# Kernel tuning notes

Hardware: AMD Instinct MI355X
Metric: run time of the kernel (lower is better)

Reference implementation:

```python
import jax, jax.numpy as jnp
import numpy as np

B, T, N, FI = 2, 16, 256, 1
H, NHEAD, L = 64, 4, 2
MID, LOW, FOUT = 32, 16, 1


def layer_norm(x, g, b, eps=1e-5):
    m = jnp.mean(x, axis=-1, keepdims=True)
    v = jnp.var(x, axis=-1, keepdims=True)
    return (x - m) / jnp.sqrt(v + eps) * g + b


def setup_inputs() -> dict:
    key = jax.random.key(0)
    ks = jax.random.split(key, 24)
    s = 0.05
    inp = {
        'x_seq': jax.random.normal(ks[0], (B, T, N, FI), jnp.float32),
        'edge_index': jax.random.randint(ks[1], (2, 16), 0, N),
        'Wi': jax.random.normal(ks[2], (FI, H), jnp.float32) * s,
        'bi': jnp.zeros((H,), jnp.float32),
        'Wqkv': jax.random.normal(ks[3], (L, H, 3 * H), jnp.float32) * s,
        'bqkv': jnp.zeros((L, 3 * H), jnp.float32),
        'Wo': jax.random.normal(ks[4], (L, H, H), jnp.float32) * s,
        'bo': jnp.zeros((L, H), jnp.float32),
        'ln1_g': jnp.ones((L, H), jnp.float32),
        'ln1_b': jnp.zeros((L, H), jnp.float32),
        'W1': jax.random.normal(ks[5], (L, H, 4 * H), jnp.float32) * s,
        'b1': jnp.zeros((L, 4 * H), jnp.float32),
        'W2': jax.random.normal(ks[6], (L, 4 * H, H), jnp.float32) * s,
        'b2': jnp.zeros((L, H), jnp.float32),
        'ln2_g': jnp.ones((L, H), jnp.float32),
        'ln2_b': jnp.zeros((L, H), jnp.float32),
        'dW1': jax.random.normal(ks[7], (H, MID), jnp.float32) * s,
        'db1': jnp.zeros((MID,), jnp.float32),
        'dW2': jax.random.normal(ks[8], (MID, LOW), jnp.float32) * s,
        'db2': jnp.zeros((LOW,), jnp.float32),
        'dW3': jax.random.normal(ks[9], (LOW, FOUT), jnp.float32) * s,
        'db3': jnp.zeros((FOUT,), jnp.float32),
    }
    return inp


def reference(x_seq, edge_index, Wi, bi, Wqkv, bqkv, Wo, bo, ln1_g, ln1_b,
              W1, b1, W2, b2, ln2_g, ln2_b, dW1, db1, dW2, db2, dW3, db3):
    b, t, n, _ = x_seq.shape
    dh = H // NHEAD
    # input projection
    x = x_seq @ Wi + bi  # [B,T,N,H]
    # sinusoidal time positional encoding (broadcast over nodes)
    pos = jnp.arange(t, dtype=jnp.float32)[:, None]
    div = jnp.exp(jnp.arange(0, H, 2, dtype=jnp.float32) * (-jnp.log(10000.0) / H))
    tp = jnp.zeros((t, H), jnp.float32)
    tp = tp.at[:, 0::2].set(jnp.sin(pos * div)).at[:, 1::2].set(jnp.cos(pos * div))
    x = x + tp[None, :, None, :]
    S = t * n
    x = x.reshape(b, S, H)
    # block-causal additive bias: position i cannot attend to strictly future timesteps
    t_idx = jnp.arange(S) // n
    bias = jnp.where(t_idx[None, :] > t_idx[:, None], -jnp.inf, 0.0).astype(x.dtype)
    inv_sqrt_dh = 1.0 / jnp.sqrt(jnp.asarray(dh, x.dtype))
    for l in range(L):
        qkv = x @ Wqkv[l] + bqkv[l]  # [B,S,3H]
        q, k, v = jnp.split(qkv, 3, axis=-1)
        q = q.reshape(b, S, NHEAD, dh).transpose(0, 2, 1, 3)
        k = k.reshape(b, S, NHEAD, dh).transpose(0, 2, 1, 3)
        v = v.reshape(b, S, NHEAD, dh).transpose(0, 2, 1, 3)
        scores = jnp.einsum('bhqd,bhkd->bhqk', q, k) * inv_sqrt_dh + bias
        attn = jax.nn.softmax(scores, axis=-1)
        o = jnp.einsum('bhqk,bhkd->bhqd', attn, v)
        o = o.transpose(0, 2, 1, 3).reshape(b, S, H)
        o = o @ Wo[l] + bo[l]
        x = layer_norm(x + o, ln1_g[l], ln1_b[l])
        f = jax.nn.relu(x @ W1[l] + b1[l]) @ W2[l] + b2[l]
        x = layer_norm(x + f, ln2_g[l], ln2_b[l])
    last = x.reshape(b, t, n, H)[:, -1]  # [B,N,H]
    h = jax.nn.relu(last @ dW1 + db1)
    h = jax.nn.relu(h @ dW2 + db2)
    return h @ dW3 + db3  # [B,N,1]
```

## Files before the change

kernel.cpp:

```cpp
#include <hip/hip_runtime.h>
#include <math.h>


namespace {
constexpr int T_ = 16, N_ = 256, S_ = 4096;
constexpr int PAIRS = 136;

constexpr size_t OFF_A    = 0;
constexpr size_t OFF_BT   = 192;
constexpr size_t OFF_XB   = 3264;
constexpr size_t OFF_ALPH = 4288;
constexpr size_t OFF_BET  = 4292;
constexpr size_t OFF_GAM  = 4356;
constexpr size_t OFF_DELT = 4420;
constexpr size_t OFF_MN   = 5444;
constexpr size_t OFF_MX   = 5476;
constexpr size_t OFF_X    = 5632;
constexpr size_t OFF_QKV  = 529920;
constexpr size_t OFF_P0   = 2102784;
constexpr size_t OFF_PM1  = 3675648;
constexpr size_t OFF_PL1  = 3708416;
constexpr size_t OFF_PA1  = 3741184;

typedef float  f32x16 __attribute__((ext_vector_type(16)));
typedef short  short8 __attribute__((ext_vector_type(8)));

__device__ inline float wave_sum(float v) {
#pragma unroll
  for (int off = 32; off > 0; off >>= 1) v += __shfl_xor(v, off, 64);
  return v;
}
__device__ inline unsigned bf16_rne(float f) {
  unsigned u = __float_as_uint(f);
  return (u + 0x7FFFu + ((u >> 16) & 1u)) >> 16;
}
__device__ inline unsigned pack2(float a, float b) {
  return bf16_rne(a) | (bf16_rne(b) << 16);
}
__device__ inline f32x16 zero16() {
  f32x16 z;
#pragma unroll
  for (int i = 0; i < 16; ++i) z[i] = 0.f;
  return z;
}
__device__ inline float pe_val(int t, int h) {
  float div = __expf((float)(h & ~1) * (-0.14391156831212787f));
  float arg = (float)t * div;
  return (h & 1) ? cosf(arg) : sinf(arg);
}

__global__ void k_setup(const float* __restrict__ x_seq,
                        const float* __restrict__ Wi, const float* __restrict__ bi,
                        const float* __restrict__ Wqkv, const float* __restrict__ bqkv,
                        float* __restrict__ A, float* __restrict__ Bt,
                        float* __restrict__ Xb,
                        float* __restrict__ ALPH, float* __restrict__ BET,
                        float* __restrict__ GAM, float* __restrict__ DELT,
                        float* __restrict__ MN, float* __restrict__ MX) {
  int t = blockIdx.x, tid = threadIdx.x;
  if (t < 16) {
    if (tid < 192) {
      float acc = bqkv[tid];
#pragma unroll 8
      for (int h = 0; h < 64; ++h)
        acc = fmaf(bi[h] + pe_val(t, h), Wqkv[h * 192 + tid], acc);
      Bt[t * 192 + tid] = acc;
    }
    if (tid < 64) Xb[t * 64 + tid] = bi[tid] + pe_val(t, tid);
  } else if (t == 16) {
    if (tid < 192) {
      float acc = 0.f;
#pragma unroll 8
      for (int h = 0; h < 64; ++h) acc = fmaf(Wi[h], Wqkv[h * 192 + tid], acc);
      A[tid] = acc;
    }
  } else if (t == 17) {
    __shared__ float sA[128];
    __shared__ float sB[16][128];
    if (tid < 128) {
      float acc = 0.f;
#pragma unroll 8
      for (int h = 0; h < 64; ++h) acc = fmaf(Wi[h], Wqkv[h * 192 + tid], acc);
      sA[tid] = acc;
    }
    {
      int tt = tid >> 4, i = tid & 15;
      float accv[8];
#pragma unroll
      for (int j = 0; j < 8; ++j) accv[j] = bqkv[i * 8 + j];
      for (int h = 0; h < 64; ++h) {
        float xb = bi[h] + pe_val(tt, h);
#pragma unroll
        for (int j = 0; j < 8; ++j)
          accv[j] = fmaf(xb, Wqkv[h * 192 + i * 8 + j], accv[j]);
      }
#pragma unroll
      for (int j = 0; j < 8; ++j) sB[tt][i * 8 + j] = accv[j];
    }
    __syncthreads();
    const float k2 = 0.36067376022224085f;
    if (tid < 4) {
      float d = 0.f;
#pragma unroll
      for (int i = 0; i < 16; ++i) d = fmaf(sA[tid * 16 + i], sA[64 + tid * 16 + i], d);
      ALPH[tid] = k2 * d;
    }
    if (tid < 64) {
      int h = tid >> 4, tp2 = tid & 15;
      float d = 0.f, g = 0.f;
#pragma unroll
      for (int i = 0; i < 16; ++i) {
        d = fmaf(sA[h * 16 + i], sB[tp2][64 + h * 16 + i], d);
        g = fmaf(sA[64 + h * 16 + i], sB[tp2][h * 16 + i], g);
      }
      BET[h * 16 + tp2] = k2 * d;
      GAM[h * 16 + tp2] = k2 * g;
    }
#pragma unroll
    for (int q = 0; q < 4; ++q) {
      int idx = tid + 256 * q;
      int h = idx >> 8, ta = (idx >> 4) & 15, tb = idx & 15;
      float d = 0.f;
#pragma unroll
      for (int i = 0; i < 16; ++i)
        d = fmaf(sB[ta][h * 16 + i], sB[tb][64 + h * 16 + i], d);
      DELT[h * 256 + ta * 16 + tb] = k2 * d;
    }
  } else {
    int g = tid >> 3, i = tid & 7;
    const float* xp = x_seq + (g >> 4) * S_ + (g & 15) * N_;
    float mn = 1e30f, mx = -1e30f;
    for (int j = i; j < 256; j += 8) {
      float v = xp[j];
      mn = fminf(mn, v); mx = fmaxf(mx, v);
    }
#pragma unroll
    for (int off = 1; off < 8; off <<= 1) {
      mn = fminf(mn, __shfl_xor(mn, off, 64));
      mx = fmaxf(mx, __shfl_xor(mx, off, 64));
    }
    if (i == 0) { MN[g] = mn; MX[g] = mx; }
  }
}

__global__ __launch_bounds__(256, 4) void k_attn0(
    const float* __restrict__ x_seq,
    const float* __restrict__ ALPH, const float* __restrict__ BET,
    const float* __restrict__ GAM, const float* __restrict__ DELT,
    const float* __restrict__ MN, const float* __restrict__ MX,
    float* __restrict__ P0) {
  __shared__ float4 xk4[64];
  int blk = blockIdx.x;
  int bh = blk / PAIRS, pair = blk % PAIRS;
  int b = bh >> 2, h = bh & 3;
  int tq = 0, p = pair;
  while (p >= tq + 1) { p -= tq + 1; ++tq; }
  int kt = p;
  int tid = threadIdx.x;
  if (tid < 64) xk4[tid] = *(const float4*)(x_seq + (size_t)(b * S_ + kt * N_) + 4 * tid);
  __syncthreads();

  float x = x_seq[b * S_ + tq * N_ + tid];
  float a = fmaf(ALPH[h], x, GAM[h * 16 + tq]);
  float xext = (a >= 0.f) ? MX[b * 16 + kt] : MN[b * 16 + kt];
  float axext = a * xext;
  float Mg = axext + fmaf(BET[h * 16 + kt], x, DELT[h * 256 + tq * 16 + kt]);
  float sp0 = 0.f, sp1 = 0.f, sp2 = 0.f, sp3 = 0.f;
  float sx0 = 0.f, sx1 = 0.f, sx2 = 0.f, sx3 = 0.f;
#pragma unroll 8
  for (int j = 0; j < 64; ++j) {
    float4 xv = xk4[j];
    float e0 = __builtin_amdgcn_exp2f(fmaf(a, xv.x, -axext));
    float e1 = __builtin_amdgcn_exp2f(fmaf(a, xv.y, -axext));
    float e2 = __builtin_amdgcn_exp2f(fmaf(a, xv.z, -axext));
    float e3 = __builtin_amdgcn_exp2f(fmaf(a, xv.w, -axext));
    sp0 += e0; sp1 += e1; sp2 += e2; sp3 += e3;
    sx0 = fmaf(xv.x, e0, sx0); sx1 = fmaf(xv.y, e1, sx1);
    sx2 = fmaf(xv.z, e2, sx2); sx3 = fmaf(xv.w, e3, sx3);
  }
  size_t pb = ((size_t)(bh * 16 + tq) * 16 + kt) * 768;
  P0[pb + tid]       = Mg;
  P0[pb + 256 + tid] = (sp0 + sp1) + (sp2 + sp3);
  P0[pb + 512 + tid] = (sx0 + sx1) + (sx2 + sx3);
}

__global__ __launch_bounds__(256, 4) void k_fused0(
    const float* __restrict__ P0, const float* __restrict__ A,
    const float* __restrict__ Bt, const float* __restrict__ Xb,
    const float* __restrict__ x_seq, const float* __restrict__ Wi,
    const float* __restrict__ Wo, const float* __restrict__ bo,
    const float* __restrict__ g1, const float* __restrict__ be1,
    const float* __restrict__ W1, const float* __restrict__ bb1,
    const float* __restrict__ W2, const float* __restrict__ bb2,
    const float* __restrict__ g2, const float* __restrict__ be2,
    const float* __restrict__ Wq1, const float* __restrict__ bq1,
    float* __restrict__ X, float* __restrict__ QKV) {
  __shared__ float os[8][64], rs[8][64], xs[8][64], x2[8][64], hs[8][256];
  int tid = threadIdx.x;
  int row0 = blockIdx.x * 8;
  int b = row0 >> 12, t = (row0 >> 8) & 15, n0 = row0 & 255;

  {
    int r = tid & 7, h = (tid >> 3) & 3, d2 = tid >> 5;
    int n = n0 + r, bh = b * 4 + h;
    float M = -INFINITY, D = 0.f, SX = 0.f, bacc0 = 0.f, bacc1 = 0.f;
    for (int kt = 0; kt <= t; ++kt) {
      size_t pb = ((size_t)(bh * 16 + t) * 16 + kt) * 768 + n;
      float mg = P0[pb], sp = P0[pb + 256], sx = P0[pb + 512];
      float mnv = fmaxf(M, mg);
      float sc = __builtin_amdgcn_exp2f(M - mnv);
      float w  = __builtin_amdgcn_exp2f(mg - mnv);
      float wsp = w * sp;
      D  = fmaf(w, sp, D * sc);
      SX = fmaf(w, sx, SX * sc);
      float2 bv = *(const float2*)(Bt + kt * 192 + 128 + h * 16 + d2 * 2);
      bacc0 = fmaf(wsp, bv.x, bacc0 * sc);
      bacc1 = fmaf(wsp, bv.y, bacc1 * sc);
      M = mnv;
    }
    float invD = 1.f / D;
    float2 av = *(const float2*)(A + 128 + h * 16 + d2 * 2);
    os[r][h * 16 + d2 * 2 + 0] = fmaf(SX, av.x, bacc0) * invD;
    os[r][h * 16 + d2 * 2 + 1] = fmaf(SX, av.y, bacc1) * invD;
  }
  {
    int idx = tid;
#pragma unroll
    for (int i = 0; i < 2; ++i, idx += 256) {
      int r = idx >> 6, cc = idx & 63;
      rs[r][cc] = fmaf(x_seq[row0 + r], Wi[cc], Xb[t * 64 + cc]);
    }
  }
  __syncthreads();

  int c = tid & 63, grp = tid >> 6;
#pragma unroll
  for (int rr = 0; rr < 2; ++rr) {
    int r = grp + 4 * rr;
    float a = bo[c];
#pragma unroll 8
    for (int k = 0; k < 64; ++k) a = fmaf(os[r][k], Wo[k * 64 + c], a);
    float val = a + rs[r][c];
    float mean = wave_sum(val) * (1.f / 64.f);
    float dv = val - mean;
    float var = wave_sum(dv * dv) * (1.f / 64.f);
    xs[r][c] = dv * rsqrtf(var + 1e-5f) * g1[c] + be1[c];
  }
  __syncthreads();

  {
    float am[8];
#pragma unroll
    for (int i = 0; i < 8; ++i) am[i] = bb1[tid];
    for (int k4 = 0; k4 < 16; ++k4) {
      float w0 = W1[(4 * k4 + 0) * 256 + tid];
      float w1v = W1[(4 * k4 + 1) * 256 + tid];
      float w2v = W1[(4 * k4 + 2) * 256 + tid];
      float w3v = W1[(4 * k4 + 3) * 256 + tid];
#pragma unroll
      for (int r = 0; r < 8; ++r) {
        float4 xv = *(const float4*)&xs[r][4 * k4];
        am[r] = fmaf(xv.x, w0, am[r]);
        am[r] = fmaf(xv.y, w1v, am[r]);
        am[r] = fmaf(xv.z, w2v, am[r]);
        am[r] = fmaf(xv.w, w3v, am[r]);
      }
    }
#pragma unroll
    for (int r = 0; r < 8; ++r) hs[r][tid] = fmaxf(am[r], 0.f);
  }
  __syncthreads();

  {
    float a0 = bb2[c], a1 = bb2[c];
    for (int k4 = 0; k4 < 64; ++k4) {
      float w0 = W2[(4 * k4 + 0) * 64 + c];
      float w1v = W2[(4 * k4 + 1) * 64 + c];
      float w2v = W2[(4 * k4 + 2) * 64 + c];
      float w3v = W2[(4 * k4 + 3) * 64 + c];
      float4 h0 = *(const float4*)&hs[grp][4 * k4];
      float4 h1 = *(const float4*)&hs[grp + 4][4 * k4];
      a0 = fmaf(h0.x, w0, a0); a0 = fmaf(h0.y, w1v, a0);
      a0 = fmaf(h0.z, w2v, a0); a0 = fmaf(h0.w, w3v, a0);
      a1 = fmaf(h1.x, w0, a1); a1 = fmaf(h1.y, w1v, a1);
      a1 = fmaf(h1.z, w2v, a1); a1 = fmaf(h1.w, w3v, a1);
    }
    float av[2] = {a0, a1};
#pragma unroll
    for (int rr = 0; rr < 2; ++rr) {
      int r = grp + 4 * rr;
      float val = av[rr] + xs[r][c];
      float mean = wave_sum(val) * (1.f / 64.f);
      float dv = val - mean;
      float var = wave_sum(dv * dv) * (1.f / 64.f);
      float xn = dv * rsqrtf(var + 1e-5f) * g2[c] + be2[c];
      x2[r][c] = xn;
      if (t == 15) X[(size_t)(row0 + r) * 64 + c] = xn;
    }
  }
  __syncthreads();

  {
    int ncol = (t == 15) ? 192 : 128;
    int cb = (t == 15) ? 0 : 64;
    if (tid < ncol) {
      int col = cb + tid;
      float acc[8];
#pragma unroll
      for (int r = 0; r < 8; ++r) acc[r] = bq1[col];
      for (int k4 = 0; k4 < 16; ++k4) {
        float w0 = Wq1[(4 * k4 + 0) * 192 + col];
        float w1v = Wq1[(4 * k4 + 1) * 192 + col];
        float w2v = Wq1[(4 * k4 + 2) * 192 + col];
        float w3v = Wq1[(4 * k4 + 3) * 192 + col];
#pragma unroll
        for (int r = 0; r < 8; ++r) {
          float4 xv = *(const float4*)&x2[r][4 * k4];
          acc[r] = fmaf(xv.x, w0, acc[r]);
          acc[r] = fmaf(xv.y, w1v, acc[r]);
          acc[r] = fmaf(xv.z, w2v, acc[r]);
          acc[r] = fmaf(xv.w, w3v, acc[r]);
        }
      }
#pragma unroll
      for (int r = 0; r < 8; ++r)
        QKV[(size_t)(row0 + r) * 192 + col] = acc[r];
    }
  }
}

__global__ __launch_bounds__(256, 4) void k_attn1(const float* __restrict__ QKV,
    float* __restrict__ PM, float* __restrict__ PL, float* __restrict__ PACC) {
  __shared__ short KH[2][256][8];
  __shared__ short KL[2][256][8];
  __shared__ short VT[32][264];
  int blk = blockIdx.x;
  int bh = blk >> 4, kt = blk & 15;
  const int tq = 15;
  int b = bh >> 2, h = bh & 3;
  int tid = threadIdx.x, w = tid >> 6, lane = tid & 63;
  int l31 = lane & 31, hi = lane >> 5;
  const size_t qkvbase = (size_t)b * S_ * 192;

  for (int i = tid; i < 16 * 264; i += 256) (&VT[16][0])[i] = 0;
  {
    const float* kp = QKV + qkvbase + (size_t)(kt * N_ + tid) * 192 + 64 + h * 16;
    float kf[16], vf[16];
#pragma unroll
    for (int i = 0; i < 4; ++i) {
      float4 k4 = *(const float4*)(kp + 4 * i);
      kf[4 * i] = k4.x; kf[4 * i + 1] = k4.y; kf[4 * i + 2] = k4.z; kf[4 * i + 3] = k4.w;
      float4 v4 = *(const float4*)(kp + 64 + 4 * i);
      vf[4 * i] = v4.x; vf[4 * i + 1] = v4.y; vf[4 * i + 2] = v4.z; vf[4 * i + 3] = v4.w;
    }
    short8 kh0, kh1, kl0, kl1;
#pragma unroll
    for (int i = 0; i < 8; ++i) {
      unsigned ht0 = __float_as_uint(kf[i]) & 0xFFFF0000u;
      kh0[i] = (short)(ht0 >> 16);
      kl0[i] = (short)bf16_rne(kf[i] - __uint_as_float(ht0));
      unsigned ht1 = __float_as_uint(kf[i + 8]) & 0xFFFF0000u;
      kh1[i] = (short)(ht1 >> 16);
      kl1[i] = (short)bf16_rne(kf[i + 8] - __uint_as_float(ht1));
    }
    *(short8*)&KH[0][tid][0] = kh0;
    *(short8*)&KH[1][tid][0] = kh1;
    *(short8*)&KL[0][tid][0] = kl0;
    *(short8*)&KL[1][tid][0] = kl1;
#pragma unroll
    for (int i = 0; i < 16; ++i) VT[i][tid] = (short)bf16_rne(vf[i]);
  }
  __syncthreads();

  const float cscale = 0.36067376022224085f;
  short8 Qh[2], Ql[2];
#pragma unroll
  for (int qs = 0; qs < 2; ++qs) {
    int qloc = w * 64 + qs * 32 + l31;
    const float* qp = QKV + qkvbase + (size_t)(tq * N_ + qloc) * 192 + h * 16 + 8 * hi;
    float4 a4 = *(const float4*)(qp), b4 = *(const float4*)(qp + 4);
    float qf[8] = {a4.x, a4.y, a4.z, a4.w, b4.x, b4.y, b4.z, b4.w};
#pragma unroll
    for (int i = 0; i < 8; ++i) {
      float q = qf[i] * cscale;
      unsigned ht = __float_as_uint(q) & 0xFFFF0000u;
      Qh[qs][i] = (short)(ht >> 16);
      Ql[qs][i] = (short)bf16_rne(q - __uint_as_float(ht));
    }
  }

  f32x16 O0 = zero16(), O1 = zero16();
  float m[2] = {-INFINITY, -INFINITY}, lsum[2] = {0.f, 0.f};

  for (int ks = 0; ks < 8; ++ks) {
    const short8 Kh = *(const short8*)&KH[hi][ks * 32 + l31][0];
    const short8 Kl = *(const short8*)&KL[hi][ks * 32 + l31][0];
    const short8 Va = *(const short8*)&VT[l31][ks * 32 + 8 * hi];
    const short8 Vb = *(const short8*)&VT[l31][ks * 32 + 8 * hi + 16];

#pragma unroll
    for (int qs = 0; qs < 2; ++qs) {
      f32x16 S = zero16();
      S = __builtin_amdgcn_mfma_f32_32x32x16_bf16(Kh, Qh[qs], S, 0, 0, 0);
      S = __builtin_amdgcn_mfma_f32_32x32x16_bf16(Kl, Qh[qs], S, 0, 0, 0);
      S = __builtin_amdgcn_mfma_f32_32x32x16_bf16(Kh, Ql[qs], S, 0, 0, 0);

      float pm = S[0];
#pragma unroll
      for (int r = 1; r < 16; ++r) pm = fmaxf(pm, S[r]);
      pm = fmaxf(pm, __shfl_xor(pm, 32, 64));
      float mq = m[qs];
      if (__any(pm > mq)) {
        float mn = fmaxf(mq, pm);
        float al = __builtin_amdgcn_exp2f(mq - mn);
        m[qs] = mn; mq = mn;
        lsum[qs] *= al;
        if (qs == 0) {
#pragma unroll
          for (int r = 0; r < 16; ++r) O0[r] *= al;
        } else {
#pragma unroll
          for (int r = 0; r < 16; ++r) O1[r] *= al;
        }
      }
      float pr[16], ps = 0.f;
#pragma unroll
      for (int r = 0; r < 16; ++r) {
        pr[r] = __builtin_amdgcn_exp2f(S[r] - mq);
        ps += pr[r];
      }
      lsum[qs] += ps + __shfl_xor(ps, 32, 64);

      unsigned w01 = pack2(pr[0],  pr[1]);
      unsigned w23 = pack2(pr[2],  pr[3]);
      unsigned w45 = pack2(pr[4],  pr[5]);
      unsigned w67 = pack2(pr[6],  pr[7]);
      unsigned w89 = pack2(pr[8],  pr[9]);
      unsigned wab = pack2(pr[10], pr[11]);
      unsigned wcd = pack2(pr[12], pr[13]);
      unsigned wef = pack2(pr[14], pr[15]);
      unsigned e01 = __shfl_xor(w01, 32, 64), e23 = __shfl_xor(w23, 32, 64);
      unsigned e45 = __shfl_xor(w45, 32, 64), e67 = __shfl_xor(w67, 32, 64);
      unsigned e89 = __shfl_xor(w89, 32, 64), eab = __shfl_xor(wab, 32, 64);
      unsigned ecd = __shfl_xor(wcd, 32, 64), eef = __shfl_xor(wef, 32, 64);
      union { short8 s; unsigned u[4]; } P0u, P1u;
      P0u.u[0] = hi ? e45 : w01;
      P0u.u[1] = hi ? e67 : w23;
      P0u.u[2] = hi ? w45 : e01;
      P0u.u[3] = hi ? w67 : e23;
      P1u.u[0] = hi ? ecd : w89;
      P1u.u[1] = hi ? eef : wab;
      P1u.u[2] = hi ? wcd : e89;
      P1u.u[3] = hi ? wef : eab;

      if (qs == 0) {
        O0 = __builtin_amdgcn_mfma_f32_32x32x16_bf16(Va, P0u.s, O0, 0, 0, 0);
        O0 = __builtin_amdgcn_mfma_f32_32x32x16_bf16(Vb, P1u.s, O0, 0, 0, 0);
      } else {
        O1 = __builtin_amdgcn_mfma_f32_32x32x16_bf16(Va, P0u.s, O1, 0, 0, 0);
        O1 = __builtin_amdgcn_mfma_f32_32x32x16_bf16(Vb, P1u.s, O1, 0, 0, 0);
      }
    }
  }

  int slot = blk;
#pragma unroll
  for (int qs = 0; qs < 2; ++qs) {
    int qloc = w * 64 + qs * 32 + l31;
    if (lane < 32) {
      PM[(size_t)slot * 256 + qloc] = m[qs];
      PL[(size_t)slot * 256 + qloc] = lsum[qs];
    }
    float* pa = PACC + (size_t)slot * 4096 + (size_t)qloc * 16;
    float4 lo4, hi4;
    if (qs == 0) {
      lo4 = make_float4(O0[0], O0[1], O0[2], O0[3]);
      hi4 = make_float4(O0[4], O0[5], O0[6], O0[7]);
    } else {
      lo4 = make_float4(O1[0], O1[1], O1[2], O1[3]);
      hi4 = make_float4(O1[4], O1[5], O1[6], O1[7]);
    }
    *(float4*)(pa + 4 * hi)     = lo4;
    *(float4*)(pa + 8 + 4 * hi) = hi4;
  }
}

__global__ __launch_bounds__(256, 2) void k_fused1(
    const float* __restrict__ PM1, const float* __restrict__ PL1,
    const float* __restrict__ PA1,
    const float* __restrict__ Wo, const float* __restrict__ bo,
    const float* __restrict__ g1, const float* __restrict__ be1,
    const float* __restrict__ W1, const float* __restrict__ bb1,
    const float* __restrict__ W2, const float* __restrict__ bb2,
    const float* __restrict__ g2, const float* __restrict__ be2,
    const float* __restrict__ X,
    const float* __restrict__ dW1, const float* __restrict__ db1,
    const float* __restrict__ dW2, const float* __restrict__ db2,
    const float* __restrict__ dW3, const float* __restrict__ db3,
    float* __restrict__ out) {
  __shared__ float os[4][64], rs[4][64], xs[4][64], x2[4][64], hs[4][256];
  __shared__ float h1s[4][32], h2s[4][16];
  int tid = threadIdx.x;
  int bb = blockIdx.x >> 6;
  int nbase = (blockIdx.x & 63) * 4;
  int row0 = bb * S_ + 15 * N_ + nbase;
  size_t base = (size_t)row0 * 64;

  {
    int d = tid & 15, r = (tid >> 4) & 3, h = tid >> 6;
    int n = nbase + r;
    int sb = (bb * 4 + h) * 16;
    float M = -INFINITY;
#pragma unroll
    for (int s = 0; s < 16; ++s) M = fmaxf(M, PM1[(size_t)(sb + s) * 256 + n]);
    float D = 0.f, od = 0.f;
#pragma unroll
    for (int s = 0; s < 16; ++s) {
      float wgt = __builtin_amdgcn_exp2f(PM1[(size_t)(sb + s) * 256 + n] - M);
      D = fmaf(PL1[(size_t)(sb + s) * 256 + n], wgt, D);
      od = fmaf(PA1[(size_t)(sb + s) * 4096 + (size_t)n * 16 + d], wgt, od);
    }
    os[r][h * 16 + d] = od / D;
    rs[tid >> 6][tid & 63] = X[base + tid];
  }
  __syncthreads();

  int c = tid & 63, grp = tid >> 6;
  {
    float a = bo[c];
#pragma unroll 8
    for (int k = 0; k < 64; ++k) a = fmaf(os[grp][k], Wo[k * 64 + c], a);
    float val = a + rs[grp][c];
    float mean = wave_sum(val) * (1.f / 64.f);
    float dv = val - mean;
    float var = wave_sum(dv * dv) * (1.f / 64.f);
    xs[grp][c] = dv * rsqrtf(var + 1e-5f) * g1[c] + be1[c];
  }
  __syncthreads();

  {
    float am0 = bb1[tid], am1 = am0, am2 = am0, am3 = am0;
    for (int k4 = 0; k4 < 16; ++k4) {
      float w0 = W1[(4 * k4 + 0) * 256 + tid];
      float w1v = W1[(4 * k4 + 1) * 256 + tid];
      float w2v = W1[(4 * k4 + 2) * 256 + tid];
      float w3v = W1[(4 * k4 + 3) * 256 + tid];
      float4 x0 = *(const float4*)&xs[0][4 * k4];
      float4 x1 = *(const float4*)&xs[1][4 * k4];
      float4 x2v = *(const float4*)&xs[2][4 * k4];
      float4 x3 = *(const float4*)&xs[3][4 * k4];
      am0 = fmaf(x0.x, w0, am0); am0 = fmaf(x0.y, w1v, am0);
      am0 = fmaf(x0.z, w2v, am0); am0 = fmaf(x0.w, w3v, am0);
      am1 = fmaf(x1.x, w0, am1); am1 = fmaf(x1.y, w1v, am1);
      am1 = fmaf(x1.z, w2v, am1); am1 = fmaf(x1.w, w3v, am1);
      am2 = fmaf(x2v.x, w0, am2); am2 = fmaf(x2v.y, w1v, am2);
      am2 = fmaf(x2v.z, w2v, am2); am2 = fmaf(x2v.w, w3v, am2);
      am3 = fmaf(x3.x, w0, am3); am3 = fmaf(x3.y, w1v, am3);
      am3 = fmaf(x3.z, w2v, am3); am3 = fmaf(x3.w, w3v, am3);
    }
    hs[0][tid] = fmaxf(am0, 0.f);
    hs[1][tid] = fmaxf(am1, 0.f);
    hs[2][tid] = fmaxf(am2, 0.f);
    hs[3][tid] = fmaxf(am3, 0.f);
  }
  __syncthreads();

  {
    float a = bb2[c];
    for (int k4 = 0; k4 < 64; ++k4) {
      float w0 = W2[(4 * k4 + 0) * 64 + c];
      float w1v = W2[(4 * k4 + 1) * 64 + c];
      float w2v = W2[(4 * k4 + 2) * 64 + c];
      float w3v = W2[(4 * k4 + 3) * 64 + c];
      float4 hv = *(const float4*)&hs[grp][4 * k4];
      a = fmaf(hv.x, w0, a); a = fmaf(hv.y, w1v, a);
      a = fmaf(hv.z, w2v, a); a = fmaf(hv.w, w3v, a);
    }
    float val = a + xs[grp][c];
    float mean = wave_sum(val) * (1.f / 64.f);
    float dv = val - mean;
    float var = wave_sum(dv * dv) * (1.f / 64.f);
    x2[grp][c] = dv * rsqrtf(var + 1e-5f) * g2[c] + be2[c];
  }
  __syncthreads();

  if (tid < 128) {
    int r = tid >> 5, mid = tid & 31;
    float a = db1[mid];
#pragma unroll 8
    for (int k = 0; k < 64; ++k) a = fmaf(x2[r][k], dW1[k * 32 + mid], a);
    h1s[r][mid] = fmaxf(a, 0.f);
  }
  __syncthreads();
  if (tid < 64) {
    int r = tid >> 4, low = tid & 15;
    float a = db2[low];
#pragma unroll
    for (int k = 0; k < 32; ++k) a = fmaf(h1s[r][k], dW2[k * 16 + low], a);
    h2s[r][low] = fmaxf(a, 0.f);
  }
  __syncthreads();
  if (tid < 4) {
    float a = db3[0];
#pragma unroll
    for (int k = 0; k < 16; ++k) a = fmaf(h2s[tid][k], dW3[k], a);
    out[bb * 256 + nbase + tid] = a;
  }
}

}

extern "C" void kernel_launch(void* const* d_in, const int* in_sizes, int n_in,
                              void* d_out, int out_size, void* d_ws, size_t ws_size,
                              hipStream_t stream) {
  const float* x_seq = (const float*)d_in[0];
  const float* Wi   = (const float*)d_in[2];
  const float* bi   = (const float*)d_in[3];
  const float* Wqkv = (const float*)d_in[4];
  const float* bqkv = (const float*)d_in[5];
  const float* Wo   = (const float*)d_in[6];
  const float* bo   = (const float*)d_in[7];
  const float* ln1g = (const float*)d_in[8];
  const float* ln1b = (const float*)d_in[9];
  const float* W1   = (const float*)d_in[10];
  const float* b1   = (const float*)d_in[11];
  const float* W2   = (const float*)d_in[12];
  const float* b2   = (const float*)d_in[13];
  const float* ln2g = (const float*)d_in[14];
  const float* ln2b = (const float*)d_in[15];
  const float* dW1  = (const float*)d_in[16];
  const float* db1  = (const float*)d_in[17];
  const float* dW2  = (const float*)d_in[18];
  const float* db2  = (const float*)d_in[19];
  const float* dW3  = (const float*)d_in[20];
  const float* db3  = (const float*)d_in[21];

  float* ws   = (float*)d_ws;
  float* A    = ws + OFF_A;
  float* Bt   = ws + OFF_BT;
  float* Xb   = ws + OFF_XB;
  float* ALPH = ws + OFF_ALPH;
  float* BET  = ws + OFF_BET;
  float* GAM  = ws + OFF_GAM;
  float* DELT = ws + OFF_DELT;
  float* MN   = ws + OFF_MN;
  float* MX   = ws + OFF_MX;
  float* X    = ws + OFF_X;
  float* QKV  = ws + OFF_QKV;
  float* P0   = ws + OFF_P0;
  float* PM1  = ws + OFF_PM1;
  float* PL1  = ws + OFF_PL1;
  float* PA1  = ws + OFF_PA1;

  k_setup<<<19, 256, 0, stream>>>(x_seq, Wi, bi, Wqkv, bqkv, A, Bt, Xb,
                                  ALPH, BET, GAM, DELT, MN, MX);
  k_attn0<<<8 * PAIRS, 256, 0, stream>>>(x_seq, ALPH, BET, GAM, DELT, MN, MX, P0);
  k_fused0<<<1024, 256, 0, stream>>>(P0, A, Bt, Xb, x_seq, Wi,
                                     Wo, bo, ln1g, ln1b, W1, b1, W2, b2,
                                     ln2g, ln2b, Wqkv + 64 * 192, bqkv + 192,
                                     X, QKV);
  k_attn1<<<128, 256, 0, stream>>>(QKV, PM1, PL1, PA1);
  k_fused1<<<128, 256, 0, stream>>>(PM1, PL1, PA1,
                                    Wo + 4096, bo + 64, ln1g + 64, ln1b + 64,
                                    W1 + 64 * 256, b1 + 256, W2 + 256 * 64, b2 + 64,
                                    ln2g + 64, ln2b + 64, X,
                                    dW1, db1, dW2, db2, dW3, db3, (float*)d_out);
}
```

Measured before the change: 88.77 us.

## Move fused layer-0 MLP and projections onto split-bf16 MFMA with pretransposed weights

Rewrites k_fused0 so the Wo, W1, W2 and next-layer QKV projections run as 32x32x16 bf16 MFMA tiles. Each fp32 operand is split into a high and a low bf16 part and combined with three MFMAs to keep close to fp32 accuracy. k_setup gains 48 extra blocks that transpose and split the weights into a workspace buffer. Blocks now cover 16 rows instead of 8, with half the grid and half the padded MFMA tile zeroed, and the online softmax merge becomes a two-pass max then sum. In exchange it adds weight conversion work to every call, wastes half of each 32-row tile, and lowers the occupancy target to 2.

```diff
diff --git a/kernel.cpp b/kernel.cpp
--- a/kernel.cpp
+++ b/kernel.cpp
@@ -21,6 +21,7 @@
 constexpr size_t OFF_PM1  = 3675648;
 constexpr size_t OFF_PL1  = 3708416;
 constexpr size_t OFF_PA1  = 3741184;
+constexpr size_t OFF_WT   = 4265472;
 
 typedef float  f32x16 __attribute__((ext_vector_type(16)));
 typedef short  short8 __attribute__((ext_vector_type(8)));
@@ -48,15 +49,51 @@
   float arg = (float)t * div;
   return (h & 1) ? cosf(arg) : sinf(arg);
 }
+__device__ inline float rebuild(short h, short l) {
+  return __uint_as_float(((unsigned)(unsigned short)h) << 16) +
+         __uint_as_float(((unsigned)(unsigned short)l) << 16);
+}
+__device__ __forceinline__ void split4_store(short* hp, short* lp,
+                                             float v0, float v1, float v2, float v3) {
+  unsigned u0 = __float_as_uint(v0), u1 = __float_as_uint(v1);
+  unsigned u2 = __float_as_uint(v2), u3 = __float_as_uint(v3);
+  float r0 = v0 - __uint_as_float(u0 & 0xFFFF0000u);
+  float r1 = v1 - __uint_as_float(u1 & 0xFFFF0000u);
+  float r2 = v2 - __uint_as_float(u2 & 0xFFFF0000u);
+  float r3 = v3 - __uint_as_float(u3 & 0xFFFF0000u);
+  *(uint2*)hp = make_uint2((u0 >> 16) | (u1 & 0xFFFF0000u),
+                           (u2 >> 16) | (u3 & 0xFFFF0000u));
+  *(uint2*)lp = make_uint2(pack2(r0, r1), pack2(r2, r3));
+}
+__device__ __forceinline__ f32x16 gemm_tile(
+    const short* __restrict__ Wh, const short* __restrict__ Wl, int tileRow,
+    int inDim, int nkt, const short* Bh, const short* Bl, int bstride,
+    int l31, int hi) {
+  f32x16 C = zero16();
+  for (int kt = 0; kt < nkt; ++kt) {
+    int ko = kt * 16 + 8 * hi;
+    short8 Ah = *(const short8*)&Wh[tileRow * inDim + ko];
+    short8 Al = *(const short8*)&Wl[tileRow * inDim + ko];
+    short8 Bh8 = *(const short8*)&Bh[l31 * bstride + ko];
+    short8 Bl8 = *(const short8*)&Bl[l31 * bstride + ko];
+    C = __builtin_amdgcn_mfma_f32_32x32x16_bf16(Ah, Bh8, C, 0, 0, 0);
+    C = __builtin_amdgcn_mfma_f32_32x32x16_bf16(Al, Bh8, C, 0, 0, 0);
+    C = __builtin_amdgcn_mfma_f32_32x32x16_bf16(Ah, Bl8, C, 0, 0, 0);
+  }
+  return C;
+}
 
 __global__ void k_setup(const float* __restrict__ x_seq,
                         const float* __restrict__ Wi, const float* __restrict__ bi,
                         const float* __restrict__ Wqkv, const float* __restrict__ bqkv,
+                        const float* __restrict__ Wo, const float* __restrict__ W1,
+                        const float* __restrict__ W2,
                         float* __restrict__ A, float* __restrict__ Bt,
                         float* __restrict__ Xb,
                         float* __restrict__ ALPH, float* __restrict__ BET,
                         float* __restrict__ GAM, float* __restrict__ DELT,
-                        float* __restrict__ MN, float* __restrict__ MX) {
+                        float* __restrict__ MN, float* __restrict__ MX,
+                        short* __restrict__ WT) {
   int t = blockIdx.x, tid = threadIdx.x;
   if (t < 16) {
     if (tid < 192) {
@@ -126,7 +163,7 @@
         d = fmaf(sB[ta][h * 16 + i], sB[tb][64 + h * 16 + i], d);
       DELT[h * 256 + ta * 16 + tb] = k2 * d;
     }
-  } else {
+  } else if (t == 18) {
     int g = tid >> 3, i = tid & 7;
     const float* xp = x_seq + (g >> 4) * S_ + (g & 15) * N_;
     float mn = 1e30f, mx = -1e30f;
@@ -140,6 +177,30 @@
       mx = fmaxf(mx, __shfl_xor(mx, off, 64));
     }
     if (i == 0) { MN[g] = mn; MX[g] = mx; }
+  } else {
+    int tb2 = t - 19;
+    const float* Wq1 = Wqkv + 64 * 192;
+#pragma unroll
+    for (int e = 0; e < 4; ++e) {
+      int gi = tb2 * 1024 + e * 256 + tid;
+      float v; int hdst, ldst;
+      if (gi < 4096) {
+        int o = gi >> 6, i = gi & 63; v = Wo[i * 64 + o];
+        hdst = gi; ldst = gi + 4096;
+      } else if (gi < 20480) {
+        int li = gi - 4096; int o = li >> 6, i = li & 63; v = W1[i * 256 + o];
+        hdst = 8192 + li; ldst = 24576 + li;
+      } else if (gi < 36864) {
+        int li = gi - 20480; int o = li >> 8, i = li & 255; v = W2[i * 64 + o];
+        hdst = 40960 + li; ldst = 57344 + li;
+      } else {
+        int li = gi - 36864; int o = li >> 6, i = li & 63; v = Wq1[i * 192 + o];
+        hdst = 73728 + li; ldst = 86016 + li;
+      }
+      unsigned u = __float_as_uint(v);
+      WT[hdst] = (short)(u >> 16);
+      WT[ldst] = (short)bf16_rne(v - __uint_as_float(u & 0xFFFF0000u));
+    }
   }
 }
 
@@ -184,147 +245,170 @@
   P0[pb + 512 + tid] = (sx0 + sx1) + (sx2 + sx3);
 }
 
-__global__ __launch_bounds__(256, 4) void k_fused0(
+__global__ __launch_bounds__(256, 2) void k_fused0(
     const float* __restrict__ P0, const float* __restrict__ A,
     const float* __restrict__ Bt, const float* __restrict__ Xb,
     const float* __restrict__ x_seq, const float* __restrict__ Wi,
-    const float* __restrict__ Wo, const float* __restrict__ bo,
-    const float* __restrict__ g1, const float* __restrict__ be1,
-    const float* __restrict__ W1, const float* __restrict__ bb1,
-    const float* __restrict__ W2, const float* __restrict__ bb2,
-    const float* __restrict__ g2, const float* __restrict__ be2,
-    const float* __restrict__ Wq1, const float* __restrict__ bq1,
+    const float* __restrict__ bo, const float* __restrict__ g1,
+    const float* __restrict__ be1, const float* __restrict__ bb1,
+    const float* __restrict__ bb2, const float* __restrict__ g2,
+    const float* __restrict__ be2, const float* __restrict__ bq1,
+    const short* __restrict__ WT,
     float* __restrict__ X, float* __restrict__ QKV) {
-  __shared__ float os[8][64], rs[8][64], xs[8][64], x2[8][64], hs[8][256];
+  __shared__ short qbh[32][72], qbl[32][72];
+  __shared__ short xsh[32][72], xsl[32][72];
+  __shared__ short hsh[32][264], hsl[32][264];
+  __shared__ float ys[16][68];
+
+  const short* WoTh = WT;          const short* WoTl = WT + 4096;
+  const short* W1Th = WT + 8192;   const short* W1Tl = WT + 24576;
+  const short* W2Th = WT + 40960;  const short* W2Tl = WT + 57344;
+  const short* WqTh = WT + 73728;  const short* WqTl = WT + 86016;
+
+  int blk = blockIdx.x;
+  int b = blk >> 8, t = (blk >> 4) & 15, n0 = (blk & 15) * 16;
+  int gbase = b * S_ + t * N_ + n0;
   int tid = threadIdx.x;
-  int row0 = blockIdx.x * 8;
-  int b = row0 >> 12, t = (row0 >> 8) & 15, n0 = row0 & 255;
-
-  {
-    int r = tid & 7, h = (tid >> 3) & 3, d2 = tid >> 5;
-    int n = n0 + r, bh = b * 4 + h;
-    float M = -INFINITY, D = 0.f, SX = 0.f, bacc0 = 0.f, bacc1 = 0.f;
+  int w = tid >> 6, lane = tid & 63, l31 = lane & 31, hi = lane >> 5;
+
+  for (int i = tid; i < 16 * 72; i += 256) {
+    (&qbh[16][0])[i] = 0; (&qbl[16][0])[i] = 0;
+    (&xsh[16][0])[i] = 0; (&xsl[16][0])[i] = 0;
+  }
+  for (int i = tid; i < 16 * 264; i += 256) {
+    (&hsh[16][0])[i] = 0; (&hsl[16][0])[i] = 0;
+  }
+
+  {
+    int r = tid & 15, hh = (tid >> 4) & 3, d4 = tid >> 6;
+    int n = n0 + r, bh4 = b * 4 + hh;
+    size_t pbase = ((size_t)(bh4 * 16 + t) * 16) * 768 + n;
+    float M = -INFINITY;
+    for (int kt = 0; kt <= t; ++kt)
+      M = fmaxf(M, P0[pbase + (size_t)kt * 768]);
+    float D = 0.f, SX = 0.f, c0 = 0.f, c1 = 0.f, c2 = 0.f, c3 = 0.f;
     for (int kt = 0; kt <= t; ++kt) {
-      size_t pb = ((size_t)(bh * 16 + t) * 16 + kt) * 768 + n;
-      float mg = P0[pb], sp = P0[pb + 256], sx = P0[pb + 512];
-      float mnv = fmaxf(M, mg);
-      float sc = __builtin_amdgcn_exp2f(M - mnv);
-      float w  = __builtin_amdgcn_exp2f(mg - mnv);
-      float wsp = w * sp;
-      D  = fmaf(w, sp, D * sc);
-      SX = fmaf(w, sx, SX * sc);
-      float2 bv = *(const float2*)(Bt + kt * 192 + 128 + h * 16 + d2 * 2);
-      bacc0 = fmaf(wsp, bv.x, bacc0 * sc);
-      bacc1 = fmaf(wsp, bv.y, bacc1 * sc);
-      M = mnv;
+      size_t pb = pbase + (size_t)kt * 768;
+      float wgt = __builtin_amdgcn_exp2f(P0[pb] - M);
+      float wsp = wgt * P0[pb + 256];
+      D += wsp;
+      SX = fmaf(wgt, P0[pb + 512], SX);
+      float4 bv = *(const float4*)(Bt + kt * 192 + 128 + hh * 16 + d4 * 4);
+      c0 = fmaf(wsp, bv.x, c0); c1 = fmaf(wsp, bv.y, c1);
+      c2 = fmaf(wsp, bv.z, c2); c3 = fmaf(wsp, bv.w, c3);
     }
     float invD = 1.f / D;
-    float2 av = *(const float2*)(A + 128 + h * 16 + d2 * 2);
-    os[r][h * 16 + d2 * 2 + 0] = fmaf(SX, av.x, bacc0) * invD;
-    os[r][h * 16 + d2 * 2 + 1] = fmaf(SX, av.y, bacc1) * invD;
-  }
-  {
-    int idx = tid;
-#pragma unroll
-    for (int i = 0; i < 2; ++i, idx += 256) {
-      int r = idx >> 6, cc = idx & 63;
-      rs[r][cc] = fmaf(x_seq[row0 + r], Wi[cc], Xb[t * 64 + cc]);
-    }
-  }
-  __syncthreads();
-
-  int c = tid & 63, grp = tid >> 6;
-#pragma unroll
-  for (int rr = 0; rr < 2; ++rr) {
-    int r = grp + 4 * rr;
-    float a = bo[c];
-#pragma unroll 8
-    for (int k = 0; k < 64; ++k) a = fmaf(os[r][k], Wo[k * 64 + c], a);
-    float val = a + rs[r][c];
-    float mean = wave_sum(val) * (1.f / 64.f);
-    float dv = val - mean;
-    float var = wave_sum(dv * dv) * (1.f / 64.f);
-    xs[r][c] = dv * rsqrtf(var + 1e-5f) * g1[c] + be1[c];
-  }
-  __syncthreads();
-
-  {
-    float am[8];
-#pragma unroll
-    for (int i = 0; i < 8; ++i) am[i] = bb1[tid];
-    for (int k4 = 0; k4 < 16; ++k4) {
-      float w0 = W1[(4 * k4 + 0) * 256 + tid];
-      float w1v = W1[(4 * k4 + 1) * 256 + tid];
-      float w2v = W1[(4 * k4 + 2) * 256 + tid];
-      float w3v = W1[(4 * k4 + 3) * 256 + tid];
-#pragma unroll
-      for (int r = 0; r < 8; ++r) {
-        float4 xv = *(const float4*)&xs[r][4 * k4];
-        am[r] = fmaf(xv.x, w0, am[r]);
-        am[r] = fmaf(xv.y, w1v, am[r]);
-        am[r] = fmaf(xv.z, w2v, am[r]);
-        am[r] = fmaf(xv.w, w3v, am[r]);
-      }
-    }
-#pragma unroll
-    for (int r = 0; r < 8; ++r) hs[r][tid] = fmaxf(am[r], 0.f);
-  }
-  __syncthreads();
-
-  {
-    float a0 = bb2[c], a1 = bb2[c];
-    for (int k4 = 0; k4 < 64; ++k4) {
-      float w0 = W2[(4 * k4 + 0) * 64 + c];
-      float w1v = W2[(4 * k4 + 1) * 64 + c];
-      float w2v = W2[(4 * k4 + 2) * 64 + c];
-      float w3v = W2[(4 * k4 + 3) * 64 + c];
-      float4 h0 = *(const float4*)&hs[grp][4 * k4];
-      float4 h1 = *(const float4*)&hs[grp + 4][4 * k4];
-      a0 = fmaf(h0.x, w0, a0); a0 = fmaf(h0.y, w1v, a0);
-      a0 = fmaf(h0.z, w2v, a0); a0 = fmaf(h0.w, w3v, a0);
-      a1 = fmaf(h1.x, w0, a1); a1 = fmaf(h1.y, w1v, a1);
-      a1 = fmaf(h1.z, w2v, a1); a1 = fmaf(h1.w, w3v, a1);
-    }
-    float av[2] = {a0, a1};
-#pragma unroll
-    for (int rr = 0; rr < 2; ++rr) {
-      int r = grp + 4 * rr;
-      float val = av[rr] + xs[r][c];
+    float4 av = *(const float4*)(A + 128 + hh * 16 + d4 * 4);
+    float o0 = fmaf(SX, av.x, c0) * invD;
+    float o1 = fmaf(SX, av.y, c1) * invD;
+    float o2 = fmaf(SX, av.z, c2) * invD;
+    float o3 = fmaf(SX, av.w, c3) * invD;
+    split4_store(&qbh[r][hh * 16 + d4 * 4], &qbl[r][hh * 16 + d4 * 4],
+                 o0, o1, o2, o3);
+  }
+  __syncthreads();
+
+  if (w < 2) {
+    f32x16 C = gemm_tile(WoTh, WoTl, w * 32 + l31, 64, 4,
+                         &qbh[0][0], &qbl[0][0], 72, l31, hi);
+    if (l31 < 16) {
+#pragma unroll
+      for (int g = 0; g < 4; ++g)
+        *(float4*)&ys[l31][w * 32 + g * 8 + 4 * hi] =
+            make_float4(C[4 * g], C[4 * g + 1], C[4 * g + 2], C[4 * g + 3]);
+    }
+  }
+  __syncthreads();
+
+  {
+    int c = tid & 63, grp = tid >> 6;
+    float xb_c = Xb[t * 64 + c], wi_c = Wi[c], bo_c = bo[c];
+    float g1c = g1[c], be1c = be1[c];
+#pragma unroll
+    for (int rr = 0; rr < 4; ++rr) {
+      int row = grp * 4 + rr;
+      float xv = x_seq[gbase + row];
+      float val = ys[row][c] + bo_c + fmaf(xv, wi_c, xb_c);
       float mean = wave_sum(val) * (1.f / 64.f);
       float dv = val - mean;
       float var = wave_sum(dv * dv) * (1.f / 64.f);
-      float xn = dv * rsqrtf(var + 1e-5f) * g2[c] + be2[c];
-      x2[r][c] = xn;
-      if (t == 15) X[(size_t)(row0 + r) * 64 + c] = xn;
-    }
-  }
-  __syncthreads();
-
-  {
-    int ncol = (t == 15) ? 192 : 128;
-    int cb = (t == 15) ? 0 : 64;
-    if (tid < ncol) {
-      int col = cb + tid;
-      float acc[8];
-#pragma unroll
-      for (int r = 0; r < 8; ++r) acc[r] = bq1[col];
-      for (int k4 = 0; k4 < 16; ++k4) {
-        float w0 = Wq1[(4 * k4 + 0) * 192 + col];
-        float w1v = Wq1[(4 * k4 + 1) * 192 + col];
-        float w2v = Wq1[(4 * k4 + 2) * 192 + col];
-        float w3v = Wq1[(4 * k4 + 3) * 192 + col];
-#pragma unroll
-        for (int r = 0; r < 8; ++r) {
-          float4 xv = *(const float4*)&x2[r][4 * k4];
-          acc[r] = fmaf(xv.x, w0, acc[r]);
-          acc[r] = fmaf(xv.y, w1v, acc[r]);
-          acc[r] = fmaf(xv.z, w2v, acc[r]);
-          acc[r] = fmaf(xv.w, w3v, acc[r]);
+      float xn = dv * rsqrtf(var + 1e-5f) * g1c + be1c;
+      unsigned u = __float_as_uint(xn);
+      xsh[row][c] = (short)(u >> 16);
+      xsl[row][c] = (short)bf16_rne(xn - __uint_as_float(u & 0xFFFF0000u));
+    }
+  }
+  __syncthreads();
+
+#pragma unroll
+  for (int ti = 0; ti < 2; ++ti) {
+    int tt = w + 4 * ti;
+    f32x16 C = gemm_tile(W1Th, W1Tl, tt * 32 + l31, 64, 4,
+                         &xsh[0][0], &xsl[0][0], 72, l31, hi);
+    if (l31 < 16) {
+#pragma unroll
+      for (int g = 0; g < 4; ++g) {
+        int cb = tt * 32 + g * 8 + 4 * hi;
+        float v0 = fmaxf(C[4 * g + 0] + bb1[cb + 0], 0.f);
+        float v1 = fmaxf(C[4 * g + 1] + bb1[cb + 1], 0.f);
+        float v2 = fmaxf(C[4 * g + 2] + bb1[cb + 2], 0.f);
+        float v3 = fmaxf(C[4 * g + 3] + bb1[cb + 3], 0.f);
+        split4_store(&hsh[l31][cb], &hsl[l31][cb], v0, v1, v2, v3);
+      }
+    }
+  }
+  __syncthreads();
+
+  if (w < 2) {
+    f32x16 C = gemm_tile(W2Th, W2Tl, w * 32 + l31, 256, 16,
+                         &hsh[0][0], &hsl[0][0], 264, l31, hi);
+    if (l31 < 16) {
+#pragma unroll
+      for (int g = 0; g < 4; ++g)
+        *(float4*)&ys[l31][w * 32 + g * 8 + 4 * hi] =
+            make_float4(C[4 * g], C[4 * g + 1], C[4 * g + 2], C[4 * g + 3]);
+    }
+  }
+  __syncthreads();
+
+  {
+    int c = tid & 63, grp = tid >> 6;
+    float b2c = bb2[c], g2c = g2[c], be2c = be2[c];
+#pragma unroll
+    for (int rr = 0; rr < 4; ++rr) {
+      int row = grp * 4 + rr;
+      float val = ys[row][c] + b2c + rebuild(xsh[row][c], xsl[row][c]);
+      float mean = wave_sum(val) * (1.f / 64.f);
+      float dv = val - mean;
+      float var = wave_sum(dv * dv) * (1.f / 64.f);
+      float xn = dv * rsqrtf(var + 1e-5f) * g2c + be2c;
+      unsigned u = __float_as_uint(xn);
+      qbh[row][c] = (short)(u >> 16);
+      qbl[row][c] = (short)bf16_rne(xn - __uint_as_float(u & 0xFFFF0000u));
+      if (t == 15) X[(size_t)(gbase + row) * 64 + c] = xn;
+    }
+  }
+  __syncthreads();
+
+  {
+    int tlA = (t == 15) ? w : (2 + w);
+    int ntl = (t == 15 && w < 2) ? 2 : 1;
+    for (int ti = 0; ti < ntl; ++ti) {
+      int tt = ti ? (w + 4) : tlA;
+      f32x16 C = gemm_tile(WqTh, WqTl, tt * 32 + l31, 64, 4,
+                           &qbh[0][0], &qbl[0][0], 72, l31, hi);
+      if (l31 < 16) {
+        size_t rb = (size_t)(gbase + l31) * 192;
+#pragma unroll
+        for (int g = 0; g < 4; ++g) {
+          int cb = tt * 32 + g * 8 + 4 * hi;
+          float4 o = make_float4(C[4 * g + 0] + bq1[cb + 0],
+                                 C[4 * g + 1] + bq1[cb + 1],
+                                 C[4 * g + 2] + bq1[cb + 2],
+                                 C[4 * g + 3] + bq1[cb + 3]);
+          *(float4*)&QKV[rb + cb] = o;
         }
       }
-#pragma unroll
-      for (int r = 0; r < 8; ++r)
-        QKV[(size_t)(row0 + r) * 192 + col] = acc[r];
     }
   }
 }
@@ -651,14 +735,14 @@
   float* PM1  = ws + OFF_PM1;
   float* PL1  = ws + OFF_PL1;
   float* PA1  = ws + OFF_PA1;
-
-  k_setup<<<19, 256, 0, stream>>>(x_seq, Wi, bi, Wqkv, bqkv, A, Bt, Xb,
-                                  ALPH, BET, GAM, DELT, MN, MX);
+  short* WT   = (short*)(ws + OFF_WT);
+
+  k_setup<<<67, 256, 0, stream>>>(x_seq, Wi, bi, Wqkv, bqkv, Wo, W1, W2,
+                                  A, Bt, Xb, ALPH, BET, GAM, DELT, MN, MX, WT);
   k_attn0<<<8 * PAIRS, 256, 0, stream>>>(x_seq, ALPH, BET, GAM, DELT, MN, MX, P0);
-  k_fused0<<<1024, 256, 0, stream>>>(P0, A, Bt, Xb, x_seq, Wi,
-                                     Wo, bo, ln1g, ln1b, W1, b1, W2, b2,
-                                     ln2g, ln2b, Wqkv + 64 * 192, bqkv + 192,
-                                     X, QKV);
+  k_fused0<<<512, 256, 0, stream>>>(P0, A, Bt, Xb, x_seq, Wi,
+                                    bo, ln1g, ln1b, b1, b2, ln2g, ln2b,
+                                    bqkv + 192, WT, X, QKV);
   k_attn1<<<128, 256, 0, stream>>>(QKV, PM1, PL1, PA1);
   k_fused1<<<128, 256, 0, stream>>>(PM1, PL1, PA1,
                                     Wo + 4096, bo + 64, ln1g + 64, ln1b + 64,
```

After: 86.24 us. 2.9% less time.
